# Optimization experiments

Hardware: AMD Instinct MI355X
Metric: run time of the kernel (lower is better)

## Reference

```python
import jax, jax.numpy as jnp
import numpy as np

N = 25000
E = 400000
RAW = 64
REP = 64
HID = 128
HEADS = 2
OUT = 2
NEG_SLOPE = 0.2


def setup_inputs() -> dict:
    key = jax.random.key(0)
    ks = jax.random.split(key, 16)
    d_in1 = RAW + REP
    d_h = HID * HEADS
    inp = {
        'x': jax.random.normal(ks[0], (N, RAW), jnp.float32),
        'rep': jax.random.normal(ks[1], (N, REP), jnp.float32),
        'src': jax.random.randint(ks[2], (E,), 0, N, jnp.int32),
        'dst': jax.random.randint(ks[3], (E,), 0, N, jnp.int32),
        # GATConv 1 params
        'W1': jax.random.normal(ks[4], (d_in1, d_h), jnp.float32) * (1.0 / np.sqrt(d_in1)),
        'al1': jax.random.normal(ks[5], (HEADS, HID), jnp.float32) * 0.1,
        'ar1': jax.random.normal(ks[6], (HEADS, HID), jnp.float32) * 0.1,
        'b1': jnp.zeros((HEADS, HID), jnp.float32),
        # GATConv 2 params
        'W2': jax.random.normal(ks[7], (d_h, d_h), jnp.float32) * (1.0 / np.sqrt(d_h)),
        'al2': jax.random.normal(ks[8], (HEADS, HID), jnp.float32) * 0.1,
        'ar2': jax.random.normal(ks[9], (HEADS, HID), jnp.float32) * 0.1,
        'b2': jnp.zeros((HEADS, HID), jnp.float32),
        # final edge classifier
        'fcW': jax.random.normal(ks[10], (d_h * 2, OUT), jnp.float32) * (1.0 / np.sqrt(d_h * 2)),
        'fcb': jnp.zeros((OUT,), jnp.float32),
    }
    return inp


def _gat_conv(feat, W, a_l, a_r, bias, src, dst):
    """DGL-style GATConv: proj -> edge LeakyReLU score -> per-dst softmax -> scatter-sum."""
    n = feat.shape[0]
    h = (feat @ W).reshape(n, HEADS, HID)            # [N,H,D]
    el = jnp.einsum('nhd,hd->nh', h, a_l)            # [N,H]
    er = jnp.einsum('nhd,hd->nh', h, a_r)            # [N,H]
    e = jax.nn.leaky_relu(el[src] + er[dst], NEG_SLOPE)  # [E,H]
    # numerically stable segment softmax over incoming edges of each dst node
    m = jax.ops.segment_max(e, dst, num_segments=n)      # [N,H]
    m = jnp.where(jnp.isfinite(m), m, 0.0)
    ex = jnp.exp(e - m[dst])                             # [E,H]
    s = jax.ops.segment_sum(ex, dst, num_segments=n)     # [N,H]
    alpha = ex / s[dst]                                  # [E,H]
    out = jax.ops.segment_sum(alpha[:, :, None] * h[src], dst, num_segments=n)  # [N,H,D]
    return out + bias[None, :, :]


def reference(x, rep, src, dst, W1, al1, ar1, b1, W2, al2, ar2, b2, fcW, fcb):
    feat = jnp.concatenate([x, rep], axis=-1)                       # [N, RAW+REP]
    h = _gat_conv(feat, W1, al1, ar1, b1, src, dst)                 # [N,H,D]
    h = jax.nn.relu(h.reshape(N, HEADS * HID))                      # [N, H*D]
    h = _gat_conv(h, W2, al2, ar2, b2, src, dst)                    # [N,H,D]
    h = jax.nn.relu(h.reshape(N, HEADS * HID))                      # [N, H*D]
    edge_feat = jnp.concatenate([h[src], h[dst]], axis=1)           # [E, 2*H*D]
    return edge_feat @ fcW + fcb                                    # [E, OUT]
```

## Files before the change

### kernel.cpp

```cpp
#include <hip/hip_runtime.h>
#include <hip/hip_bf16.h>

#define HEADS 2
#define HIDD  128
#define DH    256
#define NEG   0.2f
#define CAP   128

typedef _Float16 half4 __attribute__((ext_vector_type(4)));
typedef float    f32x4 __attribute__((ext_vector_type(4)));


__global__ void k_degree(const int* __restrict__ dst, int* __restrict__ deg, int E) {
    int e = blockIdx.x * blockDim.x + threadIdx.x;
    if (e < E) atomicAdd(&deg[dst[e]], 1);
}

__global__ __launch_bounds__(1024) void k_scan(const int* __restrict__ deg,
                                               int* __restrict__ row_ptr,
                                               int* __restrict__ cursor, int n) {
    __shared__ int lds[1024];
    int tid = threadIdx.x;
    int base = tid * 32;
    int local[32];
    int sum = 0;
#pragma unroll
    for (int k = 0; k < 32; ++k) {
        int i = base + k;
        int v = (i < n) ? deg[i] : 0;
        local[k] = sum;
        sum += v;
    }
    lds[tid] = sum;
    __syncthreads();
    for (int off = 1; off < 1024; off <<= 1) {
        int t = (tid >= off) ? lds[tid - off] : 0;
        __syncthreads();
        lds[tid] += t;
        __syncthreads();
    }
    int thread_off = lds[tid] - sum;
#pragma unroll
    for (int k = 0; k < 32; ++k) {
        int i = base + k;
        if (i < n) {
            int rp = thread_off + local[k];
            row_ptr[i] = rp;
            cursor[i]  = rp;
        }
    }
    if (tid == 1023) row_ptr[n] = lds[1023];
}

__global__ void k_fill(const int* __restrict__ src, const int* __restrict__ dst,
                       int* __restrict__ cursor, int* __restrict__ csr_src, int E) {
    int e = blockIdx.x * blockDim.x + threadIdx.x;
    if (e < E) {
        int pos = atomicAdd(&cursor[dst[e]], 1);
        csr_src[pos] = src[e];
    }
}


__global__ __launch_bounds__(256) void k_cvt(const float* __restrict__ x,
                                             const float* __restrict__ rep,
                                             const float* __restrict__ W1,
                                             const float* __restrict__ W2,
                                             _Float16* __restrict__ feat16,
                                             _Float16* __restrict__ W1T,
                                             _Float16* __restrict__ W2T, int N) {
    int gid = blockIdx.x * 256 + threadIdx.x;
    int featQuads = N * 32;
    if (gid < featQuads) {
        int n = gid >> 5, d = (gid & 31) * 4;
        const float* s = (d < 64) ? (x + (size_t)n * 64 + d) : (rep + (size_t)n * 64 + (d - 64));
        float4 v = *reinterpret_cast<const float4*>(s);
        half4 o = { (_Float16)v.x, (_Float16)v.y, (_Float16)v.z, (_Float16)v.w };
        *reinterpret_cast<half4*>(feat16 + (size_t)n * 128 + d) = o;
        return;
    }
    gid -= featQuads;
    if (gid < 256 * 128) {
        int n = gid >> 7, k = gid & 127;
        W1T[n * 128 + k] = (_Float16)W1[(size_t)k * 256 + n];
        return;
    }
    gid -= 256 * 128;
    if (gid < 256 * 256) {
        int n = gid >> 8, k = gid & 255;
        W2T[n * 256 + k] = (_Float16)W2[(size_t)k * 256 + n];
    }
}


#define GBM 64
#define GBN 128
#define GBK 64

template<int K>
__global__ __launch_bounds__(256) void k_gemm16(const _Float16* __restrict__ A,
                                                const _Float16* __restrict__ BT,
                                                _Float16* __restrict__ C16, int M) {
    __shared__ _Float16 As[2][GBM * GBK];
    __shared__ _Float16 Bs[2][GBN * GBK];

    int tid = threadIdx.x;
    int lane = tid & 63;
    int wave = tid >> 6;
    int row0 = blockIdx.x * GBM;
    int col0 = blockIdx.y * GBN;
    int wrow = (wave & 1) * 32;
    int wcol = (wave >> 1) * 64;

    uint4 ra[2], rb[4];
    const int am = tid >> 3;
    const int ak8 = (tid & 7) * 8;

    auto stage_load = [&](int s) {
        const _Float16* ap = A + (size_t)(row0 + am) * K + s * GBK + ak8;
        ra[0] = *reinterpret_cast<const uint4*>(ap);
        ra[1] = *reinterpret_cast<const uint4*>(ap + (size_t)32 * K);
        const _Float16* bp = BT + (size_t)(col0 + am) * K + s * GBK + ak8;
#pragma unroll
        for (int it = 0; it < 4; ++it)
            rb[it] = *reinterpret_cast<const uint4*>(bp + (size_t)(it * 32) * K);
    };
    auto stage_write = [&](int buf) {
        char* ab = (char*)As[buf];
        char* bb = (char*)Bs[buf];
#pragma unroll
        for (int it = 0; it < 2; ++it) {
            int m = am + it * 32;
            int byte = (m * 128 + ak8 * 2) ^ ((m & 7) << 4);
            *reinterpret_cast<uint4*>(ab + byte) = ra[it];
        }
#pragma unroll
        for (int it = 0; it < 4; ++it) {
            int n = am + it * 32;
            int byte = (n * 128 + ak8 * 2) ^ ((n & 7) << 4);
            *reinterpret_cast<uint4*>(bb + byte) = rb[it];
        }
    };

    f32x4 acc[2][4];
#pragma unroll
    for (int i = 0; i < 2; ++i)
#pragma unroll
        for (int j = 0; j < 4; ++j) acc[i][j] = (f32x4){0.f, 0.f, 0.f, 0.f};

    stage_load(0);
    stage_write(0);
    __syncthreads();

    const int S = K / GBK;
    for (int s = 0; s < S; ++s) {
        if (s + 1 < S) stage_load(s + 1);
        const char* ab = (const char*)As[s & 1];
        const char* bb = (const char*)Bs[s & 1];
#pragma unroll
        for (int kk = 0; kk < GBK / 16; ++kk) {
            half4 af[2], bf[4];
#pragma unroll
            for (int i = 0; i < 2; ++i) {
                int m = wrow + i * 16 + (lane & 15);
                int byte = (m * 128 + kk * 32 + (lane >> 4) * 8) ^ ((m & 7) << 4);
                af[i] = *reinterpret_cast<const half4*>(ab + byte);
            }
#pragma unroll
            for (int j = 0; j < 4; ++j) {
                int n = wcol + j * 16 + (lane & 15);
                int byte = (n * 128 + kk * 32 + (lane >> 4) * 8) ^ ((n & 7) << 4);
                bf[j] = *reinterpret_cast<const half4*>(bb + byte);
            }
#pragma unroll
            for (int i = 0; i < 2; ++i)
#pragma unroll
                for (int j = 0; j < 4; ++j)
                    acc[i][j] = __builtin_amdgcn_mfma_f32_16x16x16f16(af[i], bf[j], acc[i][j], 0, 0, 0);
        }
        if (s + 1 < S) stage_write((s + 1) & 1);
        __syncthreads();
    }

    int r4 = (lane >> 4) * 4, cl = lane & 15;
#pragma unroll
    for (int i = 0; i < 2; ++i) {
#pragma unroll
        for (int r = 0; r < 4; ++r) {
            int row = row0 + wrow + i * 16 + r4 + r;
            if (row < M) {
                _Float16* cp = C16 + (size_t)row * DH + col0 + wcol + cl;
#pragma unroll
                for (int j = 0; j < 4; ++j)
                    cp[j * 16] = (_Float16)acc[i][j][r];
            }
        }
    }
}


__global__ __launch_bounds__(256) void k_eler(const _Float16* __restrict__ h,
                                              const float* __restrict__ al,
                                              const float* __restrict__ ar,
                                              float2* __restrict__ el2,
                                              float2* __restrict__ er2, int N) {
    int w = threadIdx.x >> 6, lane = threadIdx.x & 63;
    int node = blockIdx.x * 4 + w;
    if (node >= N) return;
    uint2 u = *reinterpret_cast<const uint2*>(h + (size_t)node * DH + lane * 4);
    const _Float16* hv = reinterpret_cast<const _Float16*>(&u);
    float4 a = *reinterpret_cast<const float4*>(al + lane * 4);
    float4 r = *reinterpret_cast<const float4*>(ar + lane * 4);
    float h0 = (float)hv[0], h1 = (float)hv[1], h2 = (float)hv[2], h3 = (float)hv[3];
    float sl = h0 * a.x + h1 * a.y + h2 * a.z + h3 * a.w;
    float sr = h0 * r.x + h1 * r.y + h2 * r.z + h3 * r.w;
#pragma unroll
    for (int off = 16; off; off >>= 1) {
        sl += __shfl_xor(sl, off);
        sr += __shfl_xor(sr, off);
    }
    float el0 = __shfl(sl, 0), el1 = __shfl(sl, 32);
    float er0 = __shfl(sr, 0), er1 = __shfl(sr, 32);
    if (lane == 0) el2[node] = make_float2(el0, el1);
    if (lane == 1) er2[node] = make_float2(er0, er1);
}


__global__ __launch_bounds__(256) void k_agg(const _Float16* __restrict__ h,
                                             const float2* __restrict__ el2,
                                             const float2* __restrict__ er2,
                                             const int* __restrict__ row_ptr,
                                             const int* __restrict__ csr_src,
                                             const float* __restrict__ bias,
                                             _Float16* __restrict__ g, int N) {
    __shared__ int    s_idx[4][CAP];
    __shared__ float2 s_a[4][CAP];

    int w = threadIdx.x >> 6, lane = threadIdx.x & 63;
    int node = blockIdx.x * 4 + w;
    if (node >= N) return;
    int beg = row_ptr[node];
    int deg = row_ptr[node + 1] - beg;
    float2 er = er2[node];
    bool lo = lane < 32;

    float m0 = -__builtin_inff(), m1 = -__builtin_inff();
    for (int i = lane; i < deg; i += 64) {
        int s = csr_src[beg + i];
        float2 el = el2[s];
        float sc0 = el.x + er.x; sc0 = sc0 > 0.f ? sc0 : NEG * sc0;
        float sc1 = el.y + er.y; sc1 = sc1 > 0.f ? sc1 : NEG * sc1;
        if (i < CAP) { s_idx[w][i] = s; s_a[w][i] = make_float2(sc0, sc1); }
        m0 = fmaxf(m0, sc0);
        m1 = fmaxf(m1, sc1);
    }
#pragma unroll
    for (int off = 32; off; off >>= 1) {
        m0 = fmaxf(m0, __shfl_xor(m0, off));
        m1 = fmaxf(m1, __shfl_xor(m1, off));
    }

    float sum0 = 0.f, sum1 = 0.f;
    for (int i = lane; i < deg; i += 64) {
        float2 sc;
        if (i < CAP) sc = s_a[w][i];
        else {
            int s = csr_src[beg + i];
            float2 el = el2[s];
            sc.x = el.x + er.x; sc.x = sc.x > 0.f ? sc.x : NEG * sc.x;
            sc.y = el.y + er.y; sc.y = sc.y > 0.f ? sc.y : NEG * sc.y;
        }
        float e0 = __expf(sc.x - m0);
        float e1 = __expf(sc.y - m1);
        if (i < CAP) s_a[w][i] = make_float2(e0, e1);
        sum0 += e0;
        sum1 += e1;
    }
#pragma unroll
    for (int off = 32; off; off >>= 1) {
        sum0 += __shfl_xor(sum0, off);
        sum1 += __shfl_xor(sum1, off);
    }
    float S   = lo ? sum0 : sum1;
    float inv = S > 0.f ? 1.f / S : 0.f;
    float mh  = lo ? m0 : m1;
    float erh = lo ? er.x : er.y;

    const _Float16* hp = h + lane * 4;
    float4 acc = make_float4(0.f, 0.f, 0.f, 0.f);

#define FETCH(I, S_, A_)                                                    \
    do {                                                                     \
        int _i = (I);                                                        \
        if (_i < CAP) {                                                      \
            S_ = s_idx[w][_i];                                               \
            float2 _a2 = s_a[w][_i];                                         \
            A_ = lo ? _a2.x : _a2.y;                                         \
        } else {                                                             \
            S_ = csr_src[beg + _i];                                          \
            float2 _el = el2[S_];                                            \
            float _sc = (lo ? _el.x : _el.y) + erh;                          \
            _sc = _sc > 0.f ? _sc : NEG * _sc;                               \
            A_ = __expf(_sc - mh);                                           \
        }                                                                    \
    } while (0)

#define ACCUM(V, A_)                                                         \
    do {                                                                     \
        const _Float16* _hv = reinterpret_cast<const _Float16*>(&(V));       \
        acc.x = fmaf(A_, (float)_hv[0], acc.x);                              \
        acc.y = fmaf(A_, (float)_hv[1], acc.y);                              \
        acc.z = fmaf(A_, (float)_hv[2], acc.z);                              \
        acc.w = fmaf(A_, (float)_hv[3], acc.w);                              \
    } while (0)

    int i = 0;
    for (; i + 4 <= deg; i += 4) {
        int s0, s1, s2, s3;
        float a0, a1, a2, a3;
        FETCH(i,     s0, a0);
        FETCH(i + 1, s1, a1);
        FETCH(i + 2, s2, a2);
        FETCH(i + 3, s3, a3);
        uint2 v0 = *reinterpret_cast<const uint2*>(hp + (size_t)s0 * DH);
        uint2 v1 = *reinterpret_cast<const uint2*>(hp + (size_t)s1 * DH);
        uint2 v2 = *reinterpret_cast<const uint2*>(hp + (size_t)s2 * DH);
        uint2 v3 = *reinterpret_cast<const uint2*>(hp + (size_t)s3 * DH);
        ACCUM(v0, a0); ACCUM(v1, a1); ACCUM(v2, a2); ACCUM(v3, a3);
    }
    for (; i < deg; ++i) {
        int s;
        float a;
        FETCH(i, s, a);
        uint2 v = *reinterpret_cast<const uint2*>(hp + (size_t)s * DH);
        ACCUM(v, a);
    }
#undef FETCH
#undef ACCUM

    float4 b = *reinterpret_cast<const float4*>(bias + lane * 4);
    half4 o;
    o[0] = (_Float16)fmaxf(fmaf(acc.x, inv, b.x), 0.f);
    o[1] = (_Float16)fmaxf(fmaf(acc.y, inv, b.y), 0.f);
    o[2] = (_Float16)fmaxf(fmaf(acc.z, inv, b.z), 0.f);
    o[3] = (_Float16)fmaxf(fmaf(acc.w, inv, b.w), 0.f);
    *reinterpret_cast<half4*>(g + (size_t)node * DH + lane * 4) = o;
}


__global__ __launch_bounds__(256) void k_proj(const _Float16* __restrict__ g2,
                                              const float* __restrict__ fcW,
                                              float* __restrict__ p, int n) {
    int gid = blockIdx.x * blockDim.x + threadIdx.x;
    int wid = gid >> 6;
    int lane = threadIdx.x & 63;
    if (wid >= n) return;
    uint2 u = *reinterpret_cast<const uint2*>(g2 + (size_t)wid * DH + lane * 4);
    const _Float16* hv = reinterpret_cast<const _Float16*>(&u);
    float a0 = 0.f, a1 = 0.f, a2 = 0.f, a3 = 0.f;
#pragma unroll
    for (int t = 0; t < 4; ++t) {
        int d = lane * 4 + t;
        float v = (float)hv[t];
        float2 wt = *reinterpret_cast<const float2*>(&fcW[d * 2]);
        float2 wb = *reinterpret_cast<const float2*>(&fcW[(DH + d) * 2]);
        a0 = fmaf(v, wt.x, a0);
        a1 = fmaf(v, wt.y, a1);
        a2 = fmaf(v, wb.x, a2);
        a3 = fmaf(v, wb.y, a3);
    }
#pragma unroll
    for (int off = 32; off; off >>= 1) {
        a0 += __shfl_xor(a0, off);
        a1 += __shfl_xor(a1, off);
        a2 += __shfl_xor(a2, off);
        a3 += __shfl_xor(a3, off);
    }
    if (lane == 0) {
        float4 v = make_float4(a0, a1, a2, a3);
        *reinterpret_cast<float4*>(&p[(size_t)wid * 4]) = v;
    }
}

__global__ void k_edgeout(const float* __restrict__ p,
                          const int* __restrict__ src,
                          const int* __restrict__ dst,
                          const float* __restrict__ fcb,
                          float* __restrict__ out, int E) {
    int e = blockIdx.x * blockDim.x + threadIdx.x;
    if (e >= E) return;
    int s = src[e], d = dst[e];
    float2 ps = *reinterpret_cast<const float2*>(&p[(size_t)s * 4]);
    float2 pd = *reinterpret_cast<const float2*>(&p[(size_t)d * 4 + 2]);
    float2 o;
    o.x = ps.x + pd.x + fcb[0];
    o.y = ps.y + pd.y + fcb[1];
    *reinterpret_cast<float2*>(&out[(size_t)e * 2]) = o;
}


extern "C" void kernel_launch(void* const* d_in, const int* in_sizes, int n_in,
                              void* d_out, int out_size, void* d_ws, size_t ws_size,
                              hipStream_t stream) {
    const float* x   = (const float*)d_in[0];
    const float* rep = (const float*)d_in[1];
    const int*   src = (const int*)d_in[2];
    const int*   dst = (const int*)d_in[3];
    const float* W1  = (const float*)d_in[4];
    const float* al1 = (const float*)d_in[5];
    const float* ar1 = (const float*)d_in[6];
    const float* b1  = (const float*)d_in[7];
    const float* W2  = (const float*)d_in[8];
    const float* al2 = (const float*)d_in[9];
    const float* ar2 = (const float*)d_in[10];
    const float* b2  = (const float*)d_in[11];
    const float* fcW = (const float*)d_in[12];
    const float* fcb = (const float*)d_in[13];
    float* out = (float*)d_out;

    int N = in_sizes[0] / 64;
    int E = in_sizes[2];

    char* ws = (char*)d_ws;
    size_t off = 0;
    auto alloc = [&](size_t bytes) -> void* {
        void* ptr = ws + off;
        off = (off + bytes + 255) & ~(size_t)255;
        return ptr;
    };
    int*       deg     = (int*)alloc((size_t)N * 4);
    int*       row_ptr = (int*)alloc((size_t)(N + 1) * 4);
    int*       cursor  = (int*)alloc((size_t)N * 4);
    int*       csr_src = (int*)alloc((size_t)E * 4);
    _Float16*  feat16  = (_Float16*)alloc((size_t)N * 128 * 2);
    _Float16*  W1T     = (_Float16*)alloc((size_t)256 * 128 * 2);
    _Float16*  W2T     = (_Float16*)alloc((size_t)256 * 256 * 2);
    _Float16*  h16     = (_Float16*)alloc((size_t)N * DH * 2);
    _Float16*  g16     = (_Float16*)alloc((size_t)N * DH * 2);
    float2*    el2     = (float2*)alloc((size_t)N * 8);
    float2*    er2     = (float2*)alloc((size_t)N * 8);
    float*     p       = (float*)alloc((size_t)N * 4 * 4);
    (void)alloc(65536);

    hipMemsetAsync(deg, 0, (size_t)N * 4, stream);

    int eb = (E + 255) / 256;
    int nb4 = (N + 3) / 4;
    int cvt_blocks = (N * 32 + 256 * 128 + 256 * 256 + 255) / 256;

    k_cvt<<<cvt_blocks, 256, 0, stream>>>(x, rep, W1, W2, feat16, W1T, W2T, N);
    k_degree<<<eb, 256, 0, stream>>>(dst, deg, E);
    k_scan<<<1, 1024, 0, stream>>>(deg, row_ptr, cursor, N);
    k_fill<<<eb, 256, 0, stream>>>(src, dst, cursor, csr_src, E);

    dim3 ggrid((N + GBM - 1) / GBM, DH / GBN);
    k_gemm16<128><<<ggrid, 256, 0, stream>>>(feat16, W1T, h16, N);
    k_eler<<<nb4, 256, 0, stream>>>(h16, al1, ar1, el2, er2, N);
    k_agg<<<nb4, 256, 0, stream>>>(h16, el2, er2, row_ptr, csr_src, b1, g16, N);
    k_gemm16<256><<<ggrid, 256, 0, stream>>>(g16, W2T, h16, N);
    k_eler<<<nb4, 256, 0, stream>>>(h16, al2, ar2, el2, er2, N);
    k_agg<<<nb4, 256, 0, stream>>>(h16, el2, er2, row_ptr, csr_src, b2, g16, N);
    k_proj<<<(N * 64 + 255) / 256, 256, 0, stream>>>(g16, fcW, p, N);
    k_edgeout<<<eb, 256, 0, stream>>>(p, src, dst, fcb, out, E);
}
```

Before: 316.7 us.

## Fuse attention-logit computation into GEMM epilogue and merge degree count into prep

The GEMM epilogue now stages the output tile through LDS, writes it back with coalesced 16-byte stores, and computes per-head el/er dot products from the staged tile. This removes the separate k_eler kernel and its reread of h. The degree-counting atomics are folded into the conversion kernel, which drops one launch. The scan now uses vectorized int4 loads over a degree buffer padded to 32768 entries. The costs are extra LDS traffic and a sync in the GEMM epilogue.

```diff
diff --git a/kernel.cpp b/kernel.cpp
--- a/kernel.cpp
+++ b/kernel.cpp
@@ -11,64 +11,16 @@
 typedef float    f32x4 __attribute__((ext_vector_type(4)));
 
 
-__global__ void k_degree(const int* __restrict__ dst, int* __restrict__ deg, int E) {
-    int e = blockIdx.x * blockDim.x + threadIdx.x;
-    if (e < E) atomicAdd(&deg[dst[e]], 1);
-}
-
-__global__ __launch_bounds__(1024) void k_scan(const int* __restrict__ deg,
-                                               int* __restrict__ row_ptr,
-                                               int* __restrict__ cursor, int n) {
-    __shared__ int lds[1024];
-    int tid = threadIdx.x;
-    int base = tid * 32;
-    int local[32];
-    int sum = 0;
-#pragma unroll
-    for (int k = 0; k < 32; ++k) {
-        int i = base + k;
-        int v = (i < n) ? deg[i] : 0;
-        local[k] = sum;
-        sum += v;
-    }
-    lds[tid] = sum;
-    __syncthreads();
-    for (int off = 1; off < 1024; off <<= 1) {
-        int t = (tid >= off) ? lds[tid - off] : 0;
-        __syncthreads();
-        lds[tid] += t;
-        __syncthreads();
-    }
-    int thread_off = lds[tid] - sum;
-#pragma unroll
-    for (int k = 0; k < 32; ++k) {
-        int i = base + k;
-        if (i < n) {
-            int rp = thread_off + local[k];
-            row_ptr[i] = rp;
-            cursor[i]  = rp;
-        }
-    }
-    if (tid == 1023) row_ptr[n] = lds[1023];
-}
-
-__global__ void k_fill(const int* __restrict__ src, const int* __restrict__ dst,
-                       int* __restrict__ cursor, int* __restrict__ csr_src, int E) {
-    int e = blockIdx.x * blockDim.x + threadIdx.x;
-    if (e < E) {
-        int pos = atomicAdd(&cursor[dst[e]], 1);
-        csr_src[pos] = src[e];
-    }
-}
-
-
-__global__ __launch_bounds__(256) void k_cvt(const float* __restrict__ x,
-                                             const float* __restrict__ rep,
-                                             const float* __restrict__ W1,
-                                             const float* __restrict__ W2,
-                                             _Float16* __restrict__ feat16,
-                                             _Float16* __restrict__ W1T,
-                                             _Float16* __restrict__ W2T, int N) {
+__global__ __launch_bounds__(256) void k_prep(const float* __restrict__ x,
+                                              const float* __restrict__ rep,
+                                              const float* __restrict__ W1,
+                                              const float* __restrict__ W2,
+                                              const int* __restrict__ dst,
+                                              _Float16* __restrict__ feat16,
+                                              _Float16* __restrict__ W1T,
+                                              _Float16* __restrict__ W2T,
+                                              int* __restrict__ deg,
+                                              int N, int E) {
     int gid = blockIdx.x * 256 + threadIdx.x;
     int featQuads = N * 32;
     if (gid < featQuads) {
@@ -89,6 +41,56 @@
     if (gid < 256 * 256) {
         int n = gid >> 8, k = gid & 255;
         W2T[n * 256 + k] = (_Float16)W2[(size_t)k * 256 + n];
+        return;
+    }
+    gid -= 256 * 256;
+    if (gid < E) atomicAdd(&deg[dst[gid]], 1);
+}
+
+
+__global__ __launch_bounds__(1024) void k_scan(const int* __restrict__ deg,
+                                               int* __restrict__ row_ptr,
+                                               int* __restrict__ cursor, int n) {
+    __shared__ int lds[1024];
+    int tid = threadIdx.x;
+    int base = tid * 32;
+    int v[32];
+#pragma unroll
+    for (int k = 0; k < 8; ++k) {
+        int4 q = *reinterpret_cast<const int4*>(deg + base + k * 4);
+        v[k * 4 + 0] = q.x; v[k * 4 + 1] = q.y; v[k * 4 + 2] = q.z; v[k * 4 + 3] = q.w;
+    }
+    int local[32];
+    int sum = 0;
+#pragma unroll
+    for (int k = 0; k < 32; ++k) { local[k] = sum; sum += v[k]; }
+    lds[tid] = sum;
+    __syncthreads();
+    for (int off = 1; off < 1024; off <<= 1) {
+        int t = (tid >= off) ? lds[tid - off] : 0;
+        __syncthreads();
+        lds[tid] += t;
+        __syncthreads();
+    }
+    int thread_off = lds[tid] - sum;
+#pragma unroll
+    for (int k = 0; k < 32; ++k) {
+        int i = base + k;
+        if (i < n) {
+            int rp = thread_off + local[k];
+            row_ptr[i] = rp;
+            cursor[i]  = rp;
+        }
+    }
+    if (tid == 1023) row_ptr[n] = lds[1023];
+}
+
+__global__ void k_fill(const int* __restrict__ src, const int* __restrict__ dst,
+                       int* __restrict__ cursor, int* __restrict__ csr_src, int E) {
+    int e = blockIdx.x * blockDim.x + threadIdx.x;
+    if (e < E) {
+        int pos = atomicAdd(&cursor[dst[e]], 1);
+        csr_src[pos] = src[e];
     }
 }
 
@@ -100,7 +102,11 @@
 template<int K>
 __global__ __launch_bounds__(256) void k_gemm16(const _Float16* __restrict__ A,
                                                 const _Float16* __restrict__ BT,
-                                                _Float16* __restrict__ C16, int M) {
+                                                _Float16* __restrict__ C16,
+                                                const float* __restrict__ alp,
+                                                const float* __restrict__ arp,
+                                                float* __restrict__ el,
+                                                float* __restrict__ er, int M) {
     __shared__ _Float16 As[2][GBM * GBK];
     __shared__ _Float16 Bs[2][GBN * GBK];
 
@@ -182,47 +188,63 @@
         __syncthreads();
     }
 
-    int r4 = (lane >> 4) * 4, cl = lane & 15;
-#pragma unroll
-    for (int i = 0; i < 2; ++i) {
-#pragma unroll
-        for (int r = 0; r < 4; ++r) {
-            int row = row0 + wrow + i * 16 + r4 + r;
-            if (row < M) {
-                _Float16* cp = C16 + (size_t)row * DH + col0 + wcol + cl;
-#pragma unroll
-                for (int j = 0; j < 4; ++j)
-                    cp[j * 16] = (_Float16)acc[i][j][r];
+    char* Cs = (char*)As;
+    {
+        int r4 = (lane >> 4) * 4, cl = lane & 15;
+#pragma unroll
+        for (int i = 0; i < 2; ++i)
+#pragma unroll
+            for (int j = 0; j < 4; ++j) {
+                int col = wcol + j * 16 + cl;
+#pragma unroll
+                for (int r = 0; r < 4; ++r) {
+                    int row = wrow + i * 16 + r4 + r;
+                    int byte = (row * 256 + col * 2) ^ ((row & 7) << 4);
+                    *reinterpret_cast<_Float16*>(Cs + byte) = (_Float16)acc[i][j][r];
+                }
             }
-        }
-    }
-}
-
-
-__global__ __launch_bounds__(256) void k_eler(const _Float16* __restrict__ h,
-                                              const float* __restrict__ al,
-                                              const float* __restrict__ ar,
-                                              float2* __restrict__ el2,
-                                              float2* __restrict__ er2, int N) {
-    int w = threadIdx.x >> 6, lane = threadIdx.x & 63;
-    int node = blockIdx.x * 4 + w;
-    if (node >= N) return;
-    uint2 u = *reinterpret_cast<const uint2*>(h + (size_t)node * DH + lane * 4);
-    const _Float16* hv = reinterpret_cast<const _Float16*>(&u);
-    float4 a = *reinterpret_cast<const float4*>(al + lane * 4);
-    float4 r = *reinterpret_cast<const float4*>(ar + lane * 4);
-    float h0 = (float)hv[0], h1 = (float)hv[1], h2 = (float)hv[2], h3 = (float)hv[3];
-    float sl = h0 * a.x + h1 * a.y + h2 * a.z + h3 * a.w;
-    float sr = h0 * r.x + h1 * r.y + h2 * r.z + h3 * r.w;
-#pragma unroll
-    for (int off = 16; off; off >>= 1) {
-        sl += __shfl_xor(sl, off);
-        sr += __shfl_xor(sr, off);
-    }
-    float el0 = __shfl(sl, 0), el1 = __shfl(sl, 32);
-    float er0 = __shfl(sr, 0), er1 = __shfl(sr, 32);
-    if (lane == 0) el2[node] = make_float2(el0, el1);
-    if (lane == 1) er2[node] = make_float2(er0, er1);
+    }
+    __syncthreads();
+
+#pragma unroll
+    for (int it = 0; it < 4; ++it) {
+        int lin = tid + it * 256;
+        int row = lin >> 4, chunk = lin & 15;
+        int gr = row0 + row;
+        if (gr < M) {
+            int byte = (row * 256 + chunk * 16) ^ ((row & 7) << 4);
+            *reinterpret_cast<uint4*>(C16 + (size_t)gr * DH + col0 + chunk * 8) =
+                *reinterpret_cast<const uint4*>(Cs + byte);
+        }
+    }
+
+    {
+        int r = lane >> 2, q = lane & 3;
+        int row = wave * 16 + r;
+        const float* alg = alp + col0;
+        const float* arg = arp + col0;
+        float els = 0.f, ers = 0.f;
+#pragma unroll
+        for (int kk = 0; kk < 4; ++kk) {
+            int c0 = q * 32 + kk * 8;
+            int byte = (row * 256 + c0 * 2) ^ ((row & 7) << 4);
+            uint4 u = *reinterpret_cast<const uint4*>(Cs + byte);
+            const _Float16* hv = (const _Float16*)&u;
+#pragma unroll
+            for (int t = 0; t < 8; ++t) {
+                float hvv = (float)hv[t];
+                els = fmaf(hvv, alg[c0 + t], els);
+                ers = fmaf(hvv, arg[c0 + t], ers);
+            }
+        }
+        els += __shfl_xor(els, 1); els += __shfl_xor(els, 2);
+        ers += __shfl_xor(ers, 1); ers += __shfl_xor(ers, 2);
+        int gr = row0 + row;
+        if (q == 0 && gr < M) {
+            el[gr * 2 + blockIdx.y] = els;
+            er[gr * 2 + blockIdx.y] = ers;
+        }
+    }
 }
 
 
@@ -428,7 +450,7 @@
         off = (off + bytes + 255) & ~(size_t)255;
         return ptr;
     };
-    int*       deg     = (int*)alloc((size_t)N * 4);
+    int*       deg     = (int*)alloc((size_t)32768 * 4);
     int*       row_ptr = (int*)alloc((size_t)(N + 1) * 4);
     int*       cursor  = (int*)alloc((size_t)N * 4);
     int*       csr_src = (int*)alloc((size_t)E * 4);
@@ -437,29 +459,26 @@
     _Float16*  W2T     = (_Float16*)alloc((size_t)256 * 256 * 2);
     _Float16*  h16     = (_Float16*)alloc((size_t)N * DH * 2);
     _Float16*  g16     = (_Float16*)alloc((size_t)N * DH * 2);
-    float2*    el2     = (float2*)alloc((size_t)N * 8);
-    float2*    er2     = (float2*)alloc((size_t)N * 8);
+    float*     el      = (float*)alloc((size_t)N * 2 * 4);
+    float*     er      = (float*)alloc((size_t)N * 2 * 4);
     float*     p       = (float*)alloc((size_t)N * 4 * 4);
     (void)alloc(65536);
 
-    hipMemsetAsync(deg, 0, (size_t)N * 4, stream);
+    hipMemsetAsync(deg, 0, (size_t)32768 * 4, stream);
 
     int eb = (E + 255) / 256;
     int nb4 = (N + 3) / 4;
-    int cvt_blocks = (N * 32 + 256 * 128 + 256 * 256 + 255) / 256;
-
-    k_cvt<<<cvt_blocks, 256, 0, stream>>>(x, rep, W1, W2, feat16, W1T, W2T, N);
-    k_degree<<<eb, 256, 0, stream>>>(dst, deg, E);
+    int prep_blocks = (N * 32 + 256 * 128 + 256 * 256 + E + 255) / 256;
+
+    k_prep<<<prep_blocks, 256, 0, stream>>>(x, rep, W1, W2, dst, feat16, W1T, W2T, deg, N, E);
     k_scan<<<1, 1024, 0, stream>>>(deg, row_ptr, cursor, N);
     k_fill<<<eb, 256, 0, stream>>>(src, dst, cursor, csr_src, E);
 
     dim3 ggrid((N + GBM - 1) / GBM, DH / GBN);
-    k_gemm16<128><<<ggrid, 256, 0, stream>>>(feat16, W1T, h16, N);
-    k_eler<<<nb4, 256, 0, stream>>>(h16, al1, ar1, el2, er2, N);
-    k_agg<<<nb4, 256, 0, stream>>>(h16, el2, er2, row_ptr, csr_src, b1, g16, N);
-    k_gemm16<256><<<ggrid, 256, 0, stream>>>(g16, W2T, h16, N);
-    k_eler<<<nb4, 256, 0, stream>>>(h16, al2, ar2, el2, er2, N);
-    k_agg<<<nb4, 256, 0, stream>>>(h16, el2, er2, row_ptr, csr_src, b2, g16, N);
+    k_gemm16<128><<<ggrid, 256, 0, stream>>>(feat16, W1T, h16, al1, ar1, el, er, N);
+    k_agg<<<nb4, 256, 0, stream>>>(h16, (const float2*)el, (const float2*)er, row_ptr, csr_src, b1, g16, N);
+    k_gemm16<256><<<ggrid, 256, 0, stream>>>(g16, W2T, h16, al2, ar2, el, er, N);
+    k_agg<<<nb4, 256, 0, stream>>>(h16, (const float2*)el, (const float2*)er, row_ptr, csr_src, b2, g16, N);
     k_proj<<<(N * 64 + 255) / 256, 256, 0, stream>>>(g16, fcW, p, N);
     k_edgeout<<<eb, 256, 0, stream>>>(p, src, dst, fcb, out, E);
 }
```

Result: faster. 305.3 us (-3.6%).
